# Optimization experiments

Hardware: AMD Instinct MI355X
Metric: run time of the kernel (lower is better)

The kernel has to match this reference:

```python
import jax, jax.numpy as jnp
import numpy as np

B, S, D, H = 4, 2048, 1024, 16
HD = D // H

def setup_inputs() -> dict:
    key = jax.random.key(0)
    ks = jax.random.split(key, 5)
    s = 1.0 / np.sqrt(D)
    return {
        "x": jax.random.normal(ks[0], (B, S, D), dtype=jnp.float32),
        "Wq": jax.random.normal(ks[1], (D, D), dtype=jnp.float32) * s,
        "Wk": jax.random.normal(ks[2], (D, D), dtype=jnp.float32) * s,
        "Wv": jax.random.normal(ks[3], (D, D), dtype=jnp.float32) * s,
        "Wo": jax.random.normal(ks[4], (D, D), dtype=jnp.float32) * s,
        "bo": jnp.zeros((D,), dtype=jnp.float32),
    }

def reference(x, Wq, Wk, Wv, Wo, bo):
    b, n, _ = x.shape
    # torch Linear: x @ W.T ; split heads -> [b, h, n, hd]
    def proj(W):
        return (x @ W.T).reshape(b, n, H, HD).transpose(0, 2, 1, 3)
    q, k, v = proj(Wq), proj(Wk), proj(Wv)
    scores = jnp.einsum('bhqd,bhkd->bhqk', q, k)  # [b,h,n,n]
    causal = jnp.triu(jnp.ones((n, n), dtype=bool), k=1)
    scores = jnp.where(causal, -jnp.inf, scores)
    attn = jax.nn.softmax(scores / np.sqrt(HD), axis=-1)  # dropout p=0.0 (eval)
    ctx = jnp.einsum('bhqk,bhkd->bhqd', attn, v)
    ctx = ctx.transpose(0, 2, 1, 3).reshape(b, n, D)
    return ctx @ Wo.T + bo
```

## Files before the change

### kernel.cpp

```cpp
#include <hip/hip_runtime.h>
#include <stdint.h>
#include <cmath>

#define BATCH 4
#define SEQ   2048
#define DM    1024
#define NH    16
#define HDIM  64
#define MROWS (BATCH*SEQ)
#define NQB   16

typedef __attribute__((ext_vector_type(8)))  __bf16 bf16x8;
typedef __attribute__((ext_vector_type(8)))  unsigned short u16x8;
typedef __attribute__((ext_vector_type(4)))  float f32x4;
typedef __attribute__((ext_vector_type(16))) float f32x16;
typedef __attribute__((ext_vector_type(4)))  unsigned int u32x4;

__device__ __forceinline__ unsigned short f2bf(float f) {
  unsigned u = __float_as_uint(f);
  u = (u + 0x7FFFu + ((u >> 16) & 1u)) >> 16;
  return (unsigned short)u;
}

__device__ __forceinline__ f32x4 mfma_bf16(bf16x8 a, bf16x8 b, f32x4 c) {
  return __builtin_amdgcn_mfma_f32_16x16x32_bf16(a, b, c, 0, 0, 0);
}
__device__ __forceinline__ f32x16 mfma32(bf16x8 a, bf16x8 b, f32x16 c) {
  return __builtin_amdgcn_mfma_f32_32x32x16_bf16(a, b, c, 0, 0, 0);
}

__device__ __forceinline__ unsigned cvtpk(float lo, float hi) {
  unsigned r;
  asm("v_cvt_pk_bf16_f32 %0, %1, %2" : "=v"(r) : "v"(lo), "v"(hi));
  return r;
}
__device__ __forceinline__ void permswap(unsigned &a, unsigned &b) {
  asm volatile("v_permlane32_swap_b32 %0, %1" : "+v"(a), "+v"(b));
}
__device__ __forceinline__ float exp2v(float x) {
  float r;
  asm("v_exp_f32 %0, %1" : "=v"(r) : "v"(x));
  return r;
}
__device__ __forceinline__ f32x16 zero16() {
  f32x16 z;
#pragma unroll
  for (int i = 0; i < 16; ++i) z[i] = 0.f;
  return z;
}

typedef const __attribute__((address_space(1))) unsigned int* as1_u32p;
typedef __attribute__((address_space(3))) unsigned int* as3_u32p;

__device__ __forceinline__ void gload16(const void* g, void* l) {
  __builtin_amdgcn_global_load_lds((as1_u32p)g, (as3_u32p)l, 16, 0, 0);
}

__global__ void cvt_f32_bf16(const float* __restrict__ src,
                             unsigned short* __restrict__ dst, int n4) {
  int i = blockIdx.x * blockDim.x + threadIdx.x;
  int stride = gridDim.x * blockDim.x;
  for (; i < n4; i += stride) {
    float4 v = ((const float4*)src)[i];
    ushort4 o;
    o.x = f2bf(v.x); o.y = f2bf(v.y); o.z = f2bf(v.z); o.w = f2bf(v.w);
    ((ushort4*)dst)[i] = o;
  }
}

__global__ void cvt_w4(const float* __restrict__ s0, const float* __restrict__ s1,
                       const float* __restrict__ s2, const float* __restrict__ s3,
                       unsigned short* __restrict__ d0, unsigned short* __restrict__ d1,
                       unsigned short* __restrict__ d2, unsigned short* __restrict__ d3,
                       int n4) {
  const float* src = (blockIdx.y == 0) ? s0 : (blockIdx.y == 1) ? s1 : (blockIdx.y == 2) ? s2 : s3;
  unsigned short* dst = (blockIdx.y == 0) ? d0 : (blockIdx.y == 1) ? d1 : (blockIdx.y == 2) ? d2 : d3;
  int i = blockIdx.x * blockDim.x + threadIdx.x;
  int stride = gridDim.x * blockDim.x;
  for (; i < n4; i += stride) {
    float4 v = ((const float4*)src)[i];
    ushort4 o;
    o.x = f2bf(v.x); o.y = f2bf(v.y); o.z = f2bf(v.z); o.w = f2bf(v.w);
    ((ushort4*)dst)[i] = o;
  }
}

__device__ __forceinline__ void gemm_tile_mainloop(
    const unsigned short* __restrict__ A, const unsigned short* __restrict__ Bw,
    int rowBase, int colBase,
    unsigned short* As, unsigned short* Bs,
    f32x4 acc[4][4], int tid)
{
  const int wid = tid >> 6, lane = tid & 63;
  const int wm = wid >> 1, wn = wid & 1;

  const unsigned short* aSrc[4];
  const unsigned short* bSrc[4];
  int ldsDst[4];
#pragma unroll
  for (int j = 0; j < 4; ++j) {
    int c = j * 256 + tid;
    int row = c >> 3;
    int inB = (c & 7) * 16;
    int off = row * DM + ((inB ^ ((row & 7) << 4)) >> 1);
    aSrc[j] = A + (size_t)rowBase * DM + off;
    bSrc[j] = Bw + (size_t)colBase * DM + off;
    ldsDst[j] = (j * 256 + wid * 64) * 8;
  }

  auto stage = [&](int buf) {
#pragma unroll
    for (int j = 0; j < 4; ++j) {
      gload16(aSrc[j], As + buf * 8192 + ldsDst[j]);
      aSrc[j] += 64;
    }
#pragma unroll
    for (int j = 0; j < 4; ++j) {
      gload16(bSrc[j], Bs + buf * 8192 + ldsDst[j]);
      bSrc[j] += 64;
    }
  };

  stage(0);
  asm volatile("s_waitcnt vmcnt(0)" ::: "memory");
  __builtin_amdgcn_s_barrier();

  for (int k0 = 0; k0 < DM; k0 += 64) {
    const int cur = (k0 >> 6) & 1;
    if (k0 + 64 < DM) stage(cur ^ 1);

    const char* Ab = (const char*)As + cur * 16384;
    const char* Bb = (const char*)Bs + cur * 16384;
#pragma unroll
    for (int s2 = 0; s2 < 2; ++s2) {
      bf16x8 af[4], bfv[4];
#pragma unroll
      for (int m = 0; m < 4; ++m) {
        int row = wm * 64 + m * 16 + (lane & 15);
        int off = row * 128 + ((s2 * 64 + ((lane >> 4) * 16)) ^ ((row & 7) << 4));
        af[m] = *(const bf16x8*)(Ab + off);
      }
#pragma unroll
      for (int n = 0; n < 4; ++n) {
        int row = wn * 64 + n * 16 + (lane & 15);
        int off = row * 128 + ((s2 * 64 + ((lane >> 4) * 16)) ^ ((row & 7) << 4));
        bfv[n] = *(const bf16x8*)(Bb + off);
      }
#pragma unroll
      for (int m = 0; m < 4; ++m)
#pragma unroll
        for (int n = 0; n < 4; ++n)
          acc[m][n] = mfma_bf16(af[m], bfv[n], acc[m][n]);
    }
    asm volatile("s_waitcnt vmcnt(0)" ::: "memory");
    __builtin_amdgcn_s_barrier();
  }
}

__global__ __launch_bounds__(256, 2) void gemm_qkv(
    const unsigned short* __restrict__ xb,
    const unsigned short* __restrict__ Wqb, const unsigned short* __restrict__ Wkb,
    const unsigned short* __restrict__ Wvb,
    unsigned short* __restrict__ Qd, unsigned short* __restrict__ Kd,
    unsigned short* __restrict__ Vd)
{
  __shared__ unsigned short As[2 * 128 * 64];
  __shared__ unsigned short Bs[2 * 128 * 64];
  const int tid = threadIdx.x;
  const int z = blockIdx.z;
  const unsigned short* W = (z == 0) ? Wqb : (z == 1) ? Wkb : Wvb;
  unsigned short* dst = (z == 0) ? Qd : (z == 1) ? Kd : Vd;
  const int rowBase = blockIdx.x * 128, colBase = blockIdx.y * 128;

  f32x4 acc[4][4];
#pragma unroll
  for (int m = 0; m < 4; ++m)
#pragma unroll
    for (int n = 0; n < 4; ++n) acc[m][n] = (f32x4){0.f, 0.f, 0.f, 0.f};

  gemm_tile_mainloop(xb, W, rowBase, colBase, As, Bs, acc, tid);

  const int wid = tid >> 6, lane = tid & 63;
  const int wm = wid >> 1, wn = wid & 1;
#pragma unroll
  for (int m = 0; m < 4; ++m)
#pragma unroll
    for (int n = 0; n < 4; ++n)
#pragma unroll
      for (int r = 0; r < 4; ++r) {
        int grow = rowBase + wm * 64 + m * 16 + ((lane >> 4) * 4) + r;
        int gcol = colBase + wn * 64 + n * 16 + (lane & 15);
        int b = grow >> 11, s = grow & (SEQ - 1);
        int h = gcol >> 6, hd = gcol & 63;
        dst[(((size_t)(b * NH + h)) * SEQ + s) * HDIM + hd] = f2bf(acc[m][n][r]);
      }
}

__global__ __launch_bounds__(256, 2) void gemm_out(
    const unsigned short* __restrict__ ctx, const unsigned short* __restrict__ Wob,
    const float* __restrict__ bo, float* __restrict__ out)
{
  __shared__ unsigned short As[2 * 128 * 64];
  __shared__ unsigned short Bs[2 * 128 * 64];
  const int tid = threadIdx.x;
  const int rowBase = blockIdx.x * 128, colBase = blockIdx.y * 128;

  f32x4 acc[4][4];
#pragma unroll
  for (int m = 0; m < 4; ++m)
#pragma unroll
    for (int n = 0; n < 4; ++n) acc[m][n] = (f32x4){0.f, 0.f, 0.f, 0.f};

  gemm_tile_mainloop(ctx, Wob, rowBase, colBase, As, Bs, acc, tid);

  const int wid = tid >> 6, lane = tid & 63;
  const int wm = wid >> 1, wn = wid & 1;
#pragma unroll
  for (int m = 0; m < 4; ++m)
#pragma unroll
    for (int n = 0; n < 4; ++n)
#pragma unroll
      for (int r = 0; r < 4; ++r) {
        int grow = rowBase + wm * 64 + m * 16 + ((lane >> 4) * 4) + r;
        int gcol = colBase + wn * 64 + n * 16 + (lane & 15);
        out[(size_t)grow * DM + gcol] = acc[m][n][r] + bo[gcol];
      }
}

__global__ void transpose_v(const unsigned short* __restrict__ Vd,
                            unsigned short* __restrict__ VT)
{
  __shared__ unsigned short tile[64 * 72];
  const int tid = threadIdx.x;
  const int bh = blockIdx.y, s0 = blockIdx.x * 64;
  const unsigned short* src = Vd + (size_t)bh * SEQ * HDIM + (size_t)s0 * HDIM;
#pragma unroll
  for (int j = 0; j < 2; ++j) {
    int c = j * 256 + tid;
    int r = c >> 3, c0 = (c & 7) * 8;
    *(u16x8*)(tile + r * 72 + c0) = *(const u16x8*)(src + r * HDIM + c0);
  }
  __syncthreads();
  unsigned short* dst = VT + (size_t)bh * HDIM * SEQ + s0;
#pragma unroll
  for (int j = 0; j < 2; ++j) {
    int c = j * 256 + tid;
    int d = c >> 3, c0 = (c & 7) * 8;
    u16x8 v;
#pragma unroll
    for (int e = 0; e < 8; ++e) v[e] = tile[(c0 + e) * 72 + d];
    *(u16x8*)(dst + (size_t)d * SEQ + c0) = v;
  }
}

__global__ __launch_bounds__(256, 2) void attn_fwd3(
    const unsigned short* __restrict__ Qg, const unsigned short* __restrict__ Kg,
    const unsigned short* __restrict__ VTg, unsigned short* __restrict__ ctx)
{
  __shared__ unsigned short smem[24576];

  const int tid = threadIdx.x, wid = tid >> 6, lane = tid & 63;
  const int hi = lane >> 5, lq = lane & 31;
  const int bh = blockIdx.y;
  const unsigned short* Qp = Qg  + (size_t)bh * SEQ * HDIM;
  const unsigned short* Kp = Kg  + (size_t)bh * SEQ * HDIM;
  const unsigned short* Vp = VTg + (size_t)bh * HDIM * SEQ;
  const int b = bh >> 4, h = bh & 15;
  const float C2 = 0.18033688f;

  int sRow[2], sSwz[2], sDst[2];
#pragma unroll
  for (int j = 0; j < 2; ++j) {
    int c = j * 256 + tid;
    sRow[j] = c >> 3;
    sSwz[j] = (((c & 7) * 16) ^ ((sRow[j] & 7) << 4)) >> 1;
    sDst[j] = (j * 256 + wid * 64) * 8;
  }
  int off0[4], off1[4];
#pragma unroll
  for (int ks = 0; ks < 4; ++ks) {
    int col = ks * 32 + hi * 16;
    off0[ks] = lq * 128 + (col ^ ((lq & 7) << 4));
    off1[ks] = (lq + 32) * 128 + (col ^ ((lq & 7) << 4));
  }

  for (int half = 0; half < 2; ++half) {
    const int qb = half == 0 ? (int)blockIdx.x : (NQB - 1 - (int)blockIdx.x);
    const int qw0 = qb * 128 + wid * 32;

    const unsigned short* kSrc[2];
    const unsigned short* vSrc[2];
#pragma unroll
    for (int j = 0; j < 2; ++j) {
      kSrc[j] = Kp + (size_t)sRow[j] * HDIM + sSwz[j];
      vSrc[j] = Vp + (size_t)sRow[j] * SEQ + sSwz[j];
    }
    auto stageKV = [&](int buf) {
#pragma unroll
      for (int j = 0; j < 2; ++j) {
        gload16(kSrc[j], smem + buf * 4096 + sDst[j]);
        kSrc[j] += 64 * HDIM;
      }
#pragma unroll
      for (int j = 0; j < 2; ++j) {
        gload16(vSrc[j], smem + 12288 + buf * 4096 + sDst[j]);
        vSrc[j] += 64;
      }
    };

    bf16x8 qf[4];
    {
      const unsigned short* qrow = Qp + (size_t)(qw0 + lq) * HDIM + hi * 8;
#pragma unroll
      for (int ks = 0; ks < 4; ++ks) qf[ks] = *(const bf16x8*)(qrow + ks * 16);
    }

    f32x16 o0 = zero16(), o1 = zero16();
    float m_run = -INFINITY, l_run = 0.f, mc2 = 0.f;
    const int nt = 2 * qb + 2;

    stageKV(0); stageKV(1);
    asm volatile("s_waitcnt vmcnt(4)" ::: "memory");
    __builtin_amdgcn_s_barrier();

    for (int t = 0; t < nt; ++t) {
      const int cur = t % 3;
      const bool pf = (t + 2) < nt;
      if (pf) stageKV((t + 2) % 3);

      if (t * 64 <= qw0 + 31) {
        const char* Kl = (const char*)smem + cur * 8192;
        f32x16 s0 = zero16(), s1 = zero16();
        __builtin_amdgcn_s_setprio(1);
#pragma unroll
        for (int ks = 0; ks < 4; ++ks) {
          bf16x8 a0 = *(const bf16x8*)(Kl + off0[ks]);
          bf16x8 a1 = *(const bf16x8*)(Kl + off1[ks]);
          s0 = mfma32(a0, qf[ks], s0);
          s1 = mfma32(a1, qf[ks], s1);
        }
        __builtin_amdgcn_s_setprio(0);

        if (t * 64 + 63 > qw0) {
          const int q = qw0 + lq;
          const int kb = t * 64 + 4 * hi;
#pragma unroll
          for (int r = 0; r < 16; ++r) {
            int k0 = kb + (r & 3) + 8 * (r >> 2);
            if (k0 > q)      s0[r] = -INFINITY;
            if (k0 + 32 > q) s1[r] = -INFINITY;
          }
        }

        float pmax = fmaxf(s0[0], s0[1]);
#pragma unroll
        for (int r = 2; r < 16; r += 2) pmax = fmaxf(pmax, fmaxf(s0[r], s0[r + 1]));
#pragma unroll
        for (int r = 0; r < 16; r += 2) pmax = fmaxf(pmax, fmaxf(s1[r], s1[r + 1]));
        pmax = fmaxf(pmax, __shfl_xor(pmax, 32, 64));

        if (!__all(pmax - m_run <= 64.0f)) {
          float mn = fmaxf(m_run, pmax);
          float alpha = exp2v((m_run - mn) * C2);
          l_run *= alpha;
#pragma unroll
          for (int r = 0; r < 16; ++r) { o0[r] *= alpha; o1[r] *= alpha; }
          m_run = mn;
          mc2 = mn * C2;
        }

        float rsum = 0.f;
#pragma unroll
        for (int r = 0; r < 16; ++r) {
          float p = exp2v(__builtin_fmaf(s0[r], C2, -mc2));
          s0[r] = p; rsum += p;
        }
#pragma unroll
        for (int r = 0; r < 16; ++r) {
          float p = exp2v(__builtin_fmaf(s1[r], C2, -mc2));
          s1[r] = p; rsum += p;
        }
        rsum += __shfl_xor(rsum, 32, 64);
        l_run += rsum;

        bf16x8 pfr[4];
#pragma unroll
        for (int h2 = 0; h2 < 2; ++h2) {
          {
            unsigned va = cvtpk(s0[h2 * 8 + 0], s0[h2 * 8 + 1]);
            unsigned vb = cvtpk(s0[h2 * 8 + 4], s0[h2 * 8 + 5]);
            unsigned vc = cvtpk(s0[h2 * 8 + 2], s0[h2 * 8 + 3]);
            unsigned vd = cvtpk(s0[h2 * 8 + 6], s0[h2 * 8 + 7]);
            permswap(va, vb); permswap(vc, vd);
            u32x4 tt; tt.x = va; tt.y = vc; tt.z = vb; tt.w = vd;
            pfr[h2] = __builtin_bit_cast(bf16x8, tt);
          }
          {
            unsigned va = cvtpk(s1[h2 * 8 + 0], s1[h2 * 8 + 1]);
            unsigned vb = cvtpk(s1[h2 * 8 + 4], s1[h2 * 8 + 5]);
            unsigned vc = cvtpk(s1[h2 * 8 + 2], s1[h2 * 8 + 3]);
            unsigned vd = cvtpk(s1[h2 * 8 + 6], s1[h2 * 8 + 7]);
            permswap(va, vb); permswap(vc, vd);
            u32x4 tt; tt.x = va; tt.y = vc; tt.z = vb; tt.w = vd;
            pfr[2 + h2] = __builtin_bit_cast(bf16x8, tt);
          }
        }

        const char* Vl = (const char*)smem + 24576 + cur * 8192;
        __builtin_amdgcn_s_setprio(1);
#pragma unroll
        for (int ks = 0; ks < 4; ++ks) {
          bf16x8 va0 = *(const bf16x8*)(Vl + off0[ks]);
          bf16x8 va1 = *(const bf16x8*)(Vl + off1[ks]);
          o0 = mfma32(va0, pfr[ks], o0);
          o1 = mfma32(va1, pfr[ks], o1);
        }
        __builtin_amdgcn_s_setprio(0);
      }

      if (pf) asm volatile("s_waitcnt vmcnt(4)" ::: "memory");
      else    asm volatile("s_waitcnt vmcnt(0)" ::: "memory");
      __builtin_amdgcn_s_barrier();
    }

    const float invl = 1.0f / l_run;
    unsigned short* Ot = smem;
    const int q = wid * 32 + lq;
#pragma unroll
    for (int r2 = 0; r2 < 16; r2 += 2) {
      int d = (r2 & 3) + 8 * (r2 >> 2) + 4 * hi;
      unsigned w0 = cvtpk(o0[r2] * invl, o0[r2 + 1] * invl);
      *(unsigned*)((char*)Ot + q * 128 + ((2 * d) ^ ((q & 7) << 4))) = w0;
      int d2 = d + 32;
      unsigned w1 = cvtpk(o1[r2] * invl, o1[r2 + 1] * invl);
      *(unsigned*)((char*)Ot + q * 128 + ((2 * d2) ^ ((q & 7) << 4))) = w1;
    }
    __syncthreads();

#pragma unroll
    for (int i = 0; i < 4; ++i) {
      int idx = i * 256 + tid;
      int qq = idx >> 3, c16 = (idx & 7) * 8;
      bf16x8 v = *(const bf16x8*)((const char*)Ot + qq * 128 + ((2 * c16) ^ ((qq & 7) << 4)));
      *(bf16x8*)(ctx + ((size_t)(b * SEQ) + qb * 128 + qq) * DM + h * 64 + c16) = v;
    }
    __syncthreads();
  }
}

extern "C" void kernel_launch(void* const* d_in, const int* in_sizes, int n_in,
                              void* d_out, int out_size, void* d_ws, size_t ws_size,
                              hipStream_t stream)
{
  (void)in_sizes; (void)n_in; (void)out_size; (void)ws_size;
  const float* x  = (const float*)d_in[0];
  const float* Wq = (const float*)d_in[1];
  const float* Wk = (const float*)d_in[2];
  const float* Wv = (const float*)d_in[3];
  const float* Wo = (const float*)d_in[4];
  const float* bo = (const float*)d_in[5];
  float* out = (float*)d_out;

  char* ws = (char*)d_ws;
  unsigned short* xb  = (unsigned short*)(ws);
  unsigned short* Wqb = (unsigned short*)(ws + (size_t)16 * 1048576);
  unsigned short* Wkb = (unsigned short*)(ws + (size_t)18 * 1048576);
  unsigned short* Wvb = (unsigned short*)(ws + (size_t)20 * 1048576);
  unsigned short* Wob = (unsigned short*)(ws + (size_t)22 * 1048576);
  unsigned short* Qd  = (unsigned short*)(ws + (size_t)24 * 1048576);
  unsigned short* Kd  = (unsigned short*)(ws + (size_t)40 * 1048576);
  unsigned short* Vd  = (unsigned short*)(ws + (size_t)56 * 1048576);
  unsigned short* ctxb= (unsigned short*)(ws + (size_t)72 * 1048576);
  unsigned short* VT  = xb;

  cvt_f32_bf16<<<2048, 256, 0, stream>>>(x, xb, MROWS * DM / 4);
  cvt_w4<<<dim3(64, 4), 256, 0, stream>>>(Wq, Wk, Wv, Wo, Wqb, Wkb, Wvb, Wob, DM * DM / 4);

  gemm_qkv<<<dim3(MROWS / 128, DM / 128, 3), 256, 0, stream>>>(xb, Wqb, Wkb, Wvb, Qd, Kd, Vd);
  transpose_v<<<dim3(SEQ / 64, BATCH * NH), 256, 0, stream>>>(Vd, VT);
  attn_fwd3<<<dim3(NQB / 2, BATCH * NH), 256, 0, stream>>>(Qd, Kd, VT, ctxb);
  gemm_out<<<dim3(MROWS / 128, DM / 128, 1), 256, 0, stream>>>(ctxb, Wob, bo, out);
}
```

Before: 253.6 us.

## Split attention KV across two wave groups and single-buffer GEMM mainloop

The attention kernel now runs 512 threads per block. Two groups of four waves each process alternate 64-key tiles, staged as 128-key superstages, and their online-softmax states are merged through LDS at the end. This is meant to double the waves working on each query block and improve latency hiding. Separately, the GEMM mainloop drops double buffering for a simple load/sync/compute/sync loop with halved LDS, which likely exposes global load latency in the projection GEMMs and adds a merge step and extra syncs to attention.

After: 272.0 us. +7.3%, slower.

```diff
diff --git a/kernel.cpp b/kernel.cpp
--- a/kernel.cpp
+++ b/kernel.cpp
@@ -93,44 +93,28 @@
 {
   const int wid = tid >> 6, lane = tid & 63;
   const int wm = wid >> 1, wn = wid & 1;
-
-  const unsigned short* aSrc[4];
-  const unsigned short* bSrc[4];
-  int ldsDst[4];
-#pragma unroll
-  for (int j = 0; j < 4; ++j) {
-    int c = j * 256 + tid;
-    int row = c >> 3;
-    int inB = (c & 7) * 16;
-    int off = row * DM + ((inB ^ ((row & 7) << 4)) >> 1);
-    aSrc[j] = A + (size_t)rowBase * DM + off;
-    bSrc[j] = Bw + (size_t)colBase * DM + off;
-    ldsDst[j] = (j * 256 + wid * 64) * 8;
-  }
-
-  auto stage = [&](int buf) {
+  const unsigned short* Atile = A + (size_t)rowBase * DM;
+  const unsigned short* Btile = Bw + (size_t)colBase * DM;
+
+  for (int k0 = 0; k0 < DM; k0 += 64) {
 #pragma unroll
     for (int j = 0; j < 4; ++j) {
-      gload16(aSrc[j], As + buf * 8192 + ldsDst[j]);
-      aSrc[j] += 64;
+      int c = j * 256 + tid;
+      int row = c >> 3;
+      int inB = (c & 7) * 16;
+      int srcE = row * DM + k0 + ((inB ^ ((row & 7) << 4)) >> 1);
+      gload16(Atile + srcE, As + (size_t)(j * 256 + wid * 64) * 8);
     }
 #pragma unroll
     for (int j = 0; j < 4; ++j) {
-      gload16(bSrc[j], Bs + buf * 8192 + ldsDst[j]);
-      bSrc[j] += 64;
-    }
-  };
-
-  stage(0);
-  asm volatile("s_waitcnt vmcnt(0)" ::: "memory");
-  __builtin_amdgcn_s_barrier();
-
-  for (int k0 = 0; k0 < DM; k0 += 64) {
-    const int cur = (k0 >> 6) & 1;
-    if (k0 + 64 < DM) stage(cur ^ 1);
-
-    const char* Ab = (const char*)As + cur * 16384;
-    const char* Bb = (const char*)Bs + cur * 16384;
+      int c = j * 256 + tid;
+      int row = c >> 3;
+      int inB = (c & 7) * 16;
+      int srcE = row * DM + k0 + ((inB ^ ((row & 7) << 4)) >> 1);
+      gload16(Btile + srcE, Bs + (size_t)(j * 256 + wid * 64) * 8);
+    }
+    __syncthreads();
+
 #pragma unroll
     for (int s2 = 0; s2 < 2; ++s2) {
       bf16x8 af[4], bfv[4];
@@ -138,13 +122,13 @@
       for (int m = 0; m < 4; ++m) {
         int row = wm * 64 + m * 16 + (lane & 15);
         int off = row * 128 + ((s2 * 64 + ((lane >> 4) * 16)) ^ ((row & 7) << 4));
-        af[m] = *(const bf16x8*)(Ab + off);
+        af[m] = *(const bf16x8*)((const char*)As + off);
       }
 #pragma unroll
       for (int n = 0; n < 4; ++n) {
         int row = wn * 64 + n * 16 + (lane & 15);
         int off = row * 128 + ((s2 * 64 + ((lane >> 4) * 16)) ^ ((row & 7) << 4));
-        bfv[n] = *(const bf16x8*)(Bb + off);
+        bfv[n] = *(const bf16x8*)((const char*)Bs + off);
       }
 #pragma unroll
       for (int m = 0; m < 4; ++m)
@@ -152,8 +136,7 @@
         for (int n = 0; n < 4; ++n)
           acc[m][n] = mfma_bf16(af[m], bfv[n], acc[m][n]);
     }
-    asm volatile("s_waitcnt vmcnt(0)" ::: "memory");
-    __builtin_amdgcn_s_barrier();
+    __syncthreads();
   }
 }
 
@@ -164,8 +147,8 @@
     unsigned short* __restrict__ Qd, unsigned short* __restrict__ Kd,
     unsigned short* __restrict__ Vd)
 {
-  __shared__ unsigned short As[2 * 128 * 64];
-  __shared__ unsigned short Bs[2 * 128 * 64];
+  __shared__ unsigned short As[128 * 64];
+  __shared__ unsigned short Bs[128 * 64];
   const int tid = threadIdx.x;
   const int z = blockIdx.z;
   const unsigned short* W = (z == 0) ? Wqb : (z == 1) ? Wkb : Wvb;
@@ -200,8 +183,8 @@
     const unsigned short* __restrict__ ctx, const unsigned short* __restrict__ Wob,
     const float* __restrict__ bo, float* __restrict__ out)
 {
-  __shared__ unsigned short As[2 * 128 * 64];
-  __shared__ unsigned short Bs[2 * 128 * 64];
+  __shared__ unsigned short As[128 * 64];
+  __shared__ unsigned short Bs[128 * 64];
   const int tid = threadIdx.x;
   const int rowBase = blockIdx.x * 128, colBase = blockIdx.y * 128;
 
@@ -253,13 +236,14 @@
   }
 }
 
-__global__ __launch_bounds__(256, 2) void attn_fwd3(
+__global__ __launch_bounds__(512, 4) void attn_fwd4(
     const unsigned short* __restrict__ Qg, const unsigned short* __restrict__ Kg,
     const unsigned short* __restrict__ VTg, unsigned short* __restrict__ ctx)
 {
-  __shared__ unsigned short smem[24576];
+  __shared__ unsigned short smem[32768];
 
   const int tid = threadIdx.x, wid = tid >> 6, lane = tid & 63;
+  const int grp = wid >> 2, wq = wid & 3;
   const int hi = lane >> 5, lq = lane & 31;
   const int bh = blockIdx.y;
   const unsigned short* Qp = Qg  + (size_t)bh * SEQ * HDIM;
@@ -268,14 +252,10 @@
   const int b = bh >> 4, h = bh & 15;
   const float C2 = 0.18033688f;
 
-  int sRow[2], sSwz[2], sDst[2];
-#pragma unroll
-  for (int j = 0; j < 2; ++j) {
-    int c = j * 256 + tid;
-    sRow[j] = c >> 3;
-    sSwz[j] = (((c & 7) * 16) ^ ((sRow[j] & 7) << 4)) >> 1;
-    sDst[j] = (j * 256 + wid * 64) * 8;
-  }
+  const int sRow = tid >> 3;
+  const int sSwz = ((((tid & 7) * 16) ^ ((sRow & 7) << 4)) >> 1);
+  const int sDst = wid * 512;
+
   int off0[4], off1[4];
 #pragma unroll
   for (int ks = 0; ks < 4; ++ks) {
@@ -286,25 +266,25 @@
 
   for (int half = 0; half < 2; ++half) {
     const int qb = half == 0 ? (int)blockIdx.x : (NQB - 1 - (int)blockIdx.x);
-    const int qw0 = qb * 128 + wid * 32;
+    const int qw0 = qb * 128 + wq * 32;
 
     const unsigned short* kSrc[2];
     const unsigned short* vSrc[2];
 #pragma unroll
-    for (int j = 0; j < 2; ++j) {
-      kSrc[j] = Kp + (size_t)sRow[j] * HDIM + sSwz[j];
-      vSrc[j] = Vp + (size_t)sRow[j] * SEQ + sSwz[j];
-    }
-    auto stageKV = [&](int buf) {
-#pragma unroll
-      for (int j = 0; j < 2; ++j) {
-        gload16(kSrc[j], smem + buf * 4096 + sDst[j]);
-        kSrc[j] += 64 * HDIM;
-      }
-#pragma unroll
-      for (int j = 0; j < 2; ++j) {
-        gload16(vSrc[j], smem + 12288 + buf * 4096 + sDst[j]);
-        vSrc[j] += 64;
+    for (int p = 0; p < 2; ++p) {
+      kSrc[p] = Kp + (size_t)(p * 64 + sRow) * HDIM + sSwz;
+      vSrc[p] = Vp + (size_t)sRow * SEQ + p * 64 + sSwz;
+    }
+    auto stageSS = [&](int d) {
+#pragma unroll
+      for (int p = 0; p < 2; ++p) {
+        gload16(kSrc[p], smem + (d * 2 + p) * 4096 + sDst);
+        kSrc[p] += 128 * HDIM;
+      }
+#pragma unroll
+      for (int p = 0; p < 2; ++p) {
+        gload16(vSrc[p], smem + 16384 + (d * 2 + p) * 4096 + sDst);
+        vSrc[p] += 128;
       }
     };
 
@@ -317,19 +297,19 @@
 
     f32x16 o0 = zero16(), o1 = zero16();
     float m_run = -INFINITY, l_run = 0.f, mc2 = 0.f;
-    const int nt = 2 * qb + 2;
-
-    stageKV(0); stageKV(1);
-    asm volatile("s_waitcnt vmcnt(4)" ::: "memory");
+    const int nss = qb + 1;
+
+    stageSS(0);
+    asm volatile("s_waitcnt vmcnt(0)" ::: "memory");
     __builtin_amdgcn_s_barrier();
 
-    for (int t = 0; t < nt; ++t) {
-      const int cur = t % 3;
-      const bool pf = (t + 2) < nt;
-      if (pf) stageKV((t + 2) % 3);
-
+    for (int ts = 0; ts < nss; ++ts) {
+      const int cur = ts & 1;
+      if (ts + 1 < nss) stageSS(cur ^ 1);
+
+      const int t = 2 * ts + grp;
       if (t * 64 <= qw0 + 31) {
-        const char* Kl = (const char*)smem + cur * 8192;
+        const char* Kl = (const char*)smem + (cur * 2 + grp) * 8192;
         f32x16 s0 = zero16(), s1 = zero16();
         __builtin_amdgcn_s_setprio(1);
 #pragma unroll
@@ -406,7 +386,7 @@
           }
         }
 
-        const char* Vl = (const char*)smem + 24576 + cur * 8192;
+        const char* Vl = (const char*)smem + 32768 + (cur * 2 + grp) * 8192;
         __builtin_amdgcn_s_setprio(1);
 #pragma unroll
         for (int ks = 0; ks < 4; ++ks) {
@@ -418,28 +398,60 @@
         __builtin_amdgcn_s_setprio(0);
       }
 
-      if (pf) asm volatile("s_waitcnt vmcnt(4)" ::: "memory");
-      else    asm volatile("s_waitcnt vmcnt(0)" ::: "memory");
+      asm volatile("s_waitcnt vmcnt(0)" ::: "memory");
       __builtin_amdgcn_s_barrier();
     }
 
-    const float invl = 1.0f / l_run;
+    float* MF = (float*)smem;
+    if (grp == 1) {
+      if (hi == 0) {
+        MF[wq * 32 + lq] = m_run;
+        MF[128 + wq * 32 + lq] = l_run;
+      }
+      int base = 256 + (wq * 64 + lane) * 32;
+#pragma unroll
+      for (int r = 0; r < 16; ++r) {
+        MF[base + r] = o0[r];
+        MF[base + 16 + r] = o1[r];
+      }
+    }
+    __syncthreads();
+    float invl = 0.f;
+    if (grp == 0) {
+      float m_b = MF[wq * 32 + lq];
+      float l_b = MF[128 + wq * 32 + lq];
+      float mn = fmaxf(m_run, m_b);
+      float aA = exp2v((m_run - mn) * C2);
+      float aB = exp2v((m_b - mn) * C2);
+      l_run = l_run * aA + l_b * aB;
+      int base = 256 + (wq * 64 + lane) * 32;
+#pragma unroll
+      for (int r = 0; r < 16; ++r) {
+        o0[r] = o0[r] * aA + MF[base + r] * aB;
+        o1[r] = o1[r] * aA + MF[base + 16 + r] * aB;
+      }
+      invl = 1.0f / l_run;
+    }
+    __syncthreads();
+
     unsigned short* Ot = smem;
-    const int q = wid * 32 + lq;
-#pragma unroll
-    for (int r2 = 0; r2 < 16; r2 += 2) {
-      int d = (r2 & 3) + 8 * (r2 >> 2) + 4 * hi;
-      unsigned w0 = cvtpk(o0[r2] * invl, o0[r2 + 1] * invl);
-      *(unsigned*)((char*)Ot + q * 128 + ((2 * d) ^ ((q & 7) << 4))) = w0;
-      int d2 = d + 32;
-      unsigned w1 = cvtpk(o1[r2] * invl, o1[r2 + 1] * invl);
-      *(unsigned*)((char*)Ot + q * 128 + ((2 * d2) ^ ((q & 7) << 4))) = w1;
-    }
-    __syncthreads();
-
-#pragma unroll
-    for (int i = 0; i < 4; ++i) {
-      int idx = i * 256 + tid;
+    if (grp == 0) {
+      const int q = wq * 32 + lq;
+#pragma unroll
+      for (int r2 = 0; r2 < 16; r2 += 2) {
+        int d = (r2 & 3) + 8 * (r2 >> 2) + 4 * hi;
+        unsigned w0 = cvtpk(o0[r2] * invl, o0[r2 + 1] * invl);
+        *(unsigned*)((char*)Ot + q * 128 + ((2 * d) ^ ((q & 7) << 4))) = w0;
+        int d2 = d + 32;
+        unsigned w1 = cvtpk(o1[r2] * invl, o1[r2 + 1] * invl);
+        *(unsigned*)((char*)Ot + q * 128 + ((2 * d2) ^ ((q & 7) << 4))) = w1;
+      }
+    }
+    __syncthreads();
+
+#pragma unroll
+    for (int i = 0; i < 2; ++i) {
+      int idx = i * 512 + tid;
       int qq = idx >> 3, c16 = (idx & 7) * 8;
       bf16x8 v = *(const bf16x8*)((const char*)Ot + qq * 128 + ((2 * c16) ^ ((qq & 7) << 4)));
       *(bf16x8*)(ctx + ((size_t)(b * SEQ) + qb * 128 + qq) * DM + h * 64 + c16) = v;
@@ -478,6 +490,6 @@
 
   gemm_qkv<<<dim3(MROWS / 128, DM / 128, 3), 256, 0, stream>>>(xb, Wqb, Wkb, Wvb, Qd, Kd, Vd);
   transpose_v<<<dim3(SEQ / 64, BATCH * NH), 256, 0, stream>>>(Vd, VT);
-  attn_fwd3<<<dim3(NQB / 2, BATCH * NH), 256, 0, stream>>>(Qd, Kd, VT, ctxb);
+  attn_fwd4<<<dim3(NQB / 2, BATCH * NH), 512, 0, stream>>>(Qd, Kd, VT, ctxb);
   gemm_out<<<dim3(MROWS / 128, DM / 128, 1), 256, 0, stream>>>(ctxb, Wob, bo, out);
 }
```
